# Kernel tuning notes

Hardware: AMD Instinct MI355X
Metric: run time of the kernel (lower is better)

Reference implementation:

```python
import jax, jax.numpy as jnp
import numpy as np

VOCAB, EMB, HID, OUT = 32000, 512, 1024, 8
B, S = 128, 512


def setup_inputs() -> dict:
    key = jax.random.key(0)
    ks = jax.random.split(key, 7)
    sequence_ids = jax.random.randint(ks[0], (B, S), 0, VOCAB)
    scale = 0.02
    emb = jax.random.normal(ks[1], (VOCAB, EMB), dtype=jnp.float32) * scale
    W_ih = jax.random.normal(ks[2], (4 * HID, EMB), dtype=jnp.float32) * scale
    W_hh = jax.random.normal(ks[3], (4 * HID, HID), dtype=jnp.float32) * scale
    b = jax.random.normal(ks[4], (4 * HID,), dtype=jnp.float32) * scale
    W_out = jax.random.normal(ks[5], (OUT, HID), dtype=jnp.float32) * scale
    b_out = jax.random.normal(ks[6], (OUT,), dtype=jnp.float32) * scale
    return {"sequence_ids": sequence_ids, "emb": emb, "W_ih": W_ih, "W_hh": W_hh,
            "b": b, "W_out": W_out, "b_out": b_out}


def reference(sequence_ids, emb, W_ih, W_hh, b, W_out, b_out):
    # embedding lookup: [B, S, E]
    x = emb[sequence_ids]
    Bb = x.shape[0]
    H = W_hh.shape[1]
    # precompute input projections for all timesteps at once: [S, B, 4H]
    xg = jnp.einsum('bse,ge->sbg', x, W_ih) + b

    def step(carry, xg_t):
        h, c = carry
        gates = xg_t + h @ W_hh.T  # [B, 4H]
        i, f, g, o = jnp.split(gates, 4, axis=-1)
        c = jax.nn.sigmoid(f) * c + jax.nn.sigmoid(i) * jnp.tanh(g)
        h = jax.nn.sigmoid(o) * jnp.tanh(c)
        return (h, c), None

    h0 = jnp.zeros((Bb, H), x.dtype)
    (h_last, _), _ = jax.lax.scan(step, (h0, h0), xg)
    # classifier on last hidden state: [B, OUT]
    return h_last @ W_out.T + b_out
```

## Files before the change

kernel.cpp:

```cpp
#include <hip/hip_runtime.h>
#include <cstdint>
#include <cstddef>

#define SEQ    512
#define BATCH  128
#define EMB    512
#define HID    1024
#define KTOT   1536
#define NOUT   8

#define RG     4
#define NBQ    64
#define NBLK   (RG*NBQ)
#define ROWS   32

typedef unsigned short u16;
typedef unsigned int   u32;
typedef unsigned long long u64;
typedef __attribute__((ext_vector_type(8))) __bf16 bf16x8;
typedef __attribute__((ext_vector_type(4))) float  f32x4;
typedef __attribute__((ext_vector_type(4))) float  float4v;
typedef __attribute__((ext_vector_type(4))) u16    u16x4;

#define OFF_X    0ull
#define SZ_X     ((size_t)SEQ*BATCH*EMB*2)
#define OFF_W    (OFF_X + SZ_X)
#define SZ_W     ((size_t)4*HID*KTOT*2)
#define OFF_RING (OFF_W + SZ_W)
#define SZ_RING  ((size_t)(SEQ+1)*BATCH*HID*2)
#define OFF_CNT  (OFF_RING + SZ_RING)
#define SZ_CNT   ((size_t)16*RG*64)
#define OFF_GO   (OFF_CNT + SZ_CNT)
#define SZ_GO    ((size_t)RG*64)
#define WS_NEED  (OFF_GO + SZ_GO)

__device__ inline u16 f2b(float f) {
  uint32_t u = __builtin_bit_cast(uint32_t, f);
  u = u + 0x7FFFu + ((u >> 16) & 1u);
  return (u16)(u >> 16);
}
__device__ inline float b2f(u16 u) {
  uint32_t v = ((uint32_t)u) << 16;
  return __builtin_bit_cast(float, v);
}
__device__ inline float sigm(float x) { return 1.0f / (1.0f + __expf(-x)); }
__device__ inline float tanh_(float x) {
  x = fminf(fmaxf(x, -15.f), 15.f);
  float e = __expf(2.f * x);
  return (e - 1.f) / (e + 1.f);
}
__device__ inline f32x4 mfma16(bf16x8 a, bf16x8 b, f32x4 c) {
  return __builtin_amdgcn_mfma_f32_16x16x32_bf16(a, b, c, 0, 0, 0);
}

__global__ void embed_kernel(const int* __restrict__ ids,
                             const float* __restrict__ emb,
                             u16* __restrict__ x) {
  int bid = blockIdx.x;
  int t = bid >> 7, b = bid & 127;
  int idx = ids[b * SEQ + t];
  const float4v* src = (const float4v*)(emb + (size_t)idx * EMB);
  float4v v = src[threadIdx.x];
  u16x4 o;
  o.x = f2b(v.x); o.y = f2b(v.y); o.z = f2b(v.z); o.w = f2b(v.w);
  *(u16x4*)(x + (size_t)bid * EMB + threadIdx.x * 4) = o;
}

__global__ void wpack_kernel(const float* __restrict__ Wih,
                             const float* __restrict__ Whh,
                             u16* __restrict__ Wp) {
  int gc = blockIdx.x;
  int unit = gc >> 2, q = gc & 3;
  int row = q * HID + unit;
  u16* dst = Wp + (size_t)gc * KTOT;
  for (int k = threadIdx.x; k < KTOT; k += 256) {
    float v = (k < EMB) ? Wih[(size_t)row * EMB + k]
                        : Whh[(size_t)row * HID + (k - EMB)];
    dst[k] = f2b(v);
  }
}

__global__ __launch_bounds__(256, 1) void lstm_kernel(
    const u16* __restrict__ x,
    const u16* __restrict__ Wp,
    const float* __restrict__ bias,
    u16* __restrict__ ring,
    u32* __restrict__ cnt,
    u32* __restrict__ go)
{
  __shared__ float pacc[4][ROWS][68];

  const int tid  = threadIdx.x;
  const int bid  = blockIdx.x;
  const int rg   = bid >> 6;
  const int nb   = bid & 63;
  const int lane = tid & 63;
  const int kq   = tid >> 6;
  const int l15  = lane & 15;
  const int lhi  = lane >> 4;

  const int nxc  = (kq == 0) ? 12 : (kq == 1 ? 4 : 0);
  const int arow = rg * ROWS + l15;

  bf16x8 wreg[12][4];
  {
    const int colbase = nb * 64;
    #pragma unroll
    for (int c = 0; c < 12; ++c)
      #pragma unroll
      for (int nt = 0; nt < 4; ++nt)
        wreg[c][nt] = *(const bf16x8*)(Wp
            + (size_t)(colbase + nt * 16 + l15) * KTOT
            + kq * 384 + c * 32 + lhi * 8);
  }

  const int urow = tid >> 3;
  const int up   = tid & 7;
  const int rowg = rg * ROWS + urow;
  float bs[2][4];
  #pragma unroll
  for (int k = 0; k < 2; ++k) {
    int ug = nb * 16 + 2 * up + k;
    #pragma unroll
    for (int q = 0; q < 4; ++q) bs[k][q] = bias[q * HID + ug];
  }
  float cst[2] = {0.f, 0.f};

  u32* gol = &go[rg * 16];

  bf16x8 af[2][12];
  #pragma unroll
  for (int c = 0; c < 12; ++c)
    if (c < nxc) {
      #pragma unroll
      for (int mt = 0; mt < 2; ++mt)
        af[mt][c] = *(const bf16x8*)(x + (size_t)(arow + mt * 16) * EMB
                                     + kq * 384 + c * 32 + lhi * 8);
    }

  #pragma unroll 1
  for (int t = 0; t < SEQ; ++t) {
    f32x4 acc[2][4];
    #pragma unroll
    for (int mt = 0; mt < 2; ++mt)
      #pragma unroll
      for (int nt = 0; nt < 4; ++nt) acc[mt][nt] = (f32x4){0.f, 0.f, 0.f, 0.f};
    #pragma unroll
    for (int c = 0; c < 12; ++c)
      if (c < nxc) {
        #pragma unroll
        for (int mt = 0; mt < 2; ++mt)
          #pragma unroll
          for (int nt = 0; nt < 4; ++nt)
            acc[mt][nt] = mfma16(af[mt][c], wreg[c][nt], acc[mt][nt]);
      }

    if (t > 0) {
      if (tid == 0) {
        while (__hip_atomic_load(gol, __ATOMIC_RELAXED,
                                 __HIP_MEMORY_SCOPE_AGENT) < (u32)t)
          __builtin_amdgcn_s_sleep(1);
        __asm__ __volatile__("" ::: "memory");
      }
      __syncthreads();
    }

    {
      const u16* hb = ring + (size_t)t * (BATCH * HID);
      #pragma unroll
      for (int c = 0; c < 12; ++c)
        if (c >= nxc) {
          #pragma unroll
          for (int mt = 0; mt < 2; ++mt)
            af[mt][c] = *(const bf16x8*)(hb + (size_t)(arow + mt * 16) * HID
                                         + (kq * 384 - 512 + c * 32) + lhi * 8);
        }
    }

    {
      int tn = (t + 1 < SEQ) ? (t + 1) : t;
      const u16* xb = x + (size_t)tn * (BATCH * EMB);
      #pragma unroll
      for (int c = 0; c < 12; ++c)
        if (c < nxc) {
          #pragma unroll
          for (int mt = 0; mt < 2; ++mt)
            af[mt][c] = *(const bf16x8*)(xb + (size_t)(arow + mt * 16) * EMB
                                         + kq * 384 + c * 32 + lhi * 8);
        }
    }


    #pragma unroll
    for (int c = 0; c < 12; ++c)
      if (c >= nxc) {
        #pragma unroll
        for (int mt = 0; mt < 2; ++mt)
          #pragma unroll
          for (int nt = 0; nt < 4; ++nt)
            acc[mt][nt] = mfma16(af[mt][c], wreg[c][nt], acc[mt][nt]);
      }

    #pragma unroll
    for (int mt = 0; mt < 2; ++mt)
      #pragma unroll
      for (int nt = 0; nt < 4; ++nt)
        #pragma unroll
        for (int rr = 0; rr < 4; ++rr) {
          int row = mt * 16 + lhi * 4 + rr;
          int c   = nt * 16 + l15;
          int pc  = (c & ~7) | ((c ^ row) & 7);
          pacc[kq][row][pc] = acc[mt][nt][rr];
        }
    __syncthreads();

    {
      float s[2][4];
      #pragma unroll
      for (int k = 0; k < 2; ++k)
        #pragma unroll
        for (int q = 0; q < 4; ++q) s[k][q] = bs[k][q];
      #pragma unroll
      for (int k2 = 0; k2 < 4; ++k2)
        #pragma unroll
        for (int cl = 0; cl < 8; ++cl) {
          int pc = 8 * up + ((cl ^ urow) & 7);
          s[cl >> 2][cl & 3] += pacc[k2][urow][pc];
        }
      float hv2[2];
      #pragma unroll
      for (int k = 0; k < 2; ++k) {
        float cn = sigm(s[k][1]) * cst[k] + sigm(s[k][0]) * tanh_(s[k][2]);
        cst[k] = cn;
        hv2[k] = sigm(s[k][3]) * tanh_(cn);
      }
      u32 val = (u32)f2b(hv2[0]) | ((u32)f2b(hv2[1]) << 16);
      u32* dst = (u32*)(ring + (size_t)(t + 1) * (BATCH * HID)
                        + (size_t)rowg * HID + nb * 16 + 2 * up);
      asm volatile("global_store_dword %0, %1, off sc0 sc1 nt"
                   :: "v"(dst), "v"(val) : "memory");
    }
    asm volatile("s_waitcnt vmcnt(0)" ::: "memory");

    __syncthreads();
    if (t == SEQ - 1) break;
    if (tid == 0) {
      u32* cl_ = &cnt[((size_t)(t & 15) * RG + rg) * 16];
      u32 old = __hip_atomic_fetch_add(cl_, 1u, __ATOMIC_RELAXED,
                                       __HIP_MEMORY_SCOPE_AGENT);
      if (old == (u32)(NBQ - 1)) {
        __hip_atomic_store(cl_, 0u, __ATOMIC_RELAXED,
                           __HIP_MEMORY_SCOPE_AGENT);
        __hip_atomic_store(gol, (u32)(t + 1), __ATOMIC_RELAXED,
                           __HIP_MEMORY_SCOPE_AGENT);
      }
    }
  }
}

__global__ void head_kernel(const u16* __restrict__ h,
                            const float* __restrict__ Wout,
                            const float* __restrict__ bout,
                            float* __restrict__ out) {
  int b = blockIdx.x, l = threadIdx.x;
  float p[NOUT];
  #pragma unroll
  for (int o = 0; o < NOUT; ++o) p[o] = 0.f;
  for (int k = l; k < HID; k += 64) {
    float hv = b2f(h[(size_t)b * HID + k]);
    #pragma unroll
    for (int o = 0; o < NOUT; ++o) p[o] += hv * Wout[(size_t)o * HID + k];
  }
  #pragma unroll
  for (int o = 0; o < NOUT; ++o) {
    float v = p[o];
    #pragma unroll
    for (int off = 32; off > 0; off >>= 1) v += __shfl_down(v, off);
    if (l == 0) out[b * NOUT + o] = v + bout[o];
  }
}

__global__ void sentinel_kernel(float* out, int n) {
  int i = blockIdx.x * 256 + threadIdx.x;
  if (i < n) out[i] = 1e9f;
}

extern "C" void kernel_launch(void* const* d_in, const int* in_sizes, int n_in,
                              void* d_out, int out_size, void* d_ws, size_t ws_size,
                              hipStream_t stream) {
  const int*   ids  = (const int*)d_in[0];
  const float* emb  = (const float*)d_in[1];
  const float* Wih  = (const float*)d_in[2];
  const float* Whh  = (const float*)d_in[3];
  const float* bias = (const float*)d_in[4];
  const float* Wout = (const float*)d_in[5];
  const float* bout = (const float*)d_in[6];
  float* out = (float*)d_out;

  if (ws_size < WS_NEED) {
    sentinel_kernel<<<(out_size + 255) / 256, 256, 0, stream>>>(out, out_size);
    return;
  }

  char* ws = (char*)d_ws;
  u16* x    = (u16*)(ws + OFF_X);
  u16* Wp   = (u16*)(ws + OFF_W);
  u16* ring = (u16*)(ws + OFF_RING);
  u32* cnt  = (u32*)(ws + OFF_CNT);
  u32* go   = (u32*)(ws + OFF_GO);

  hipMemsetAsync(ring, 0, (size_t)BATCH * HID * 2, stream);
  hipMemsetAsync(cnt, 0, SZ_CNT + SZ_GO, stream);

  embed_kernel<<<SEQ * BATCH, 128, 0, stream>>>(ids, emb, x);
  wpack_kernel<<<4 * HID, 256, 0, stream>>>(Wih, Whh, Wp);

  lstm_kernel<<<NBLK, 256, 0, stream>>>(x, Wp, bias, ring, cnt, go);

  head_kernel<<<BATCH, 64, 0, stream>>>(ring + (size_t)SEQ * BATCH * HID,
                                        Wout, bout, out);
}
```

Baseline: 3.124 ms.

## Split grid barrier into sub-group counters and balance K split across waves

The per-row-group barrier counter is split into eight sub-group counters, each incremented by eight blocks. Waiters poll all eight sub-flags with one wavefront and a wave-wide vote, which is meant to cut atomic contention on a single hot counter. The K dimension is also redistributed so that each of the four waves handles 128 input columns and 256 hidden columns. Previously wave 0 did all input work and waves 2-3 did only hidden work, so this evens out the post-barrier critical path of MFMAs. The cost is more polling loads per step and a wider global load pattern per wave.

New measurement: 3.361 ms. +7.6%, slower.

```diff
diff --git a/kernel.cpp b/kernel.cpp
--- a/kernel.cpp
+++ b/kernel.cpp
@@ -13,6 +13,7 @@
 #define NBQ    64
 #define NBLK   (RG*NBQ)
 #define ROWS   32
+#define NGR    8
 
 typedef unsigned short u16;
 typedef unsigned int   u32;
@@ -29,10 +30,12 @@
 #define OFF_RING (OFF_W + SZ_W)
 #define SZ_RING  ((size_t)(SEQ+1)*BATCH*HID*2)
 #define OFF_CNT  (OFF_RING + SZ_RING)
-#define SZ_CNT   ((size_t)16*RG*64)
-#define OFF_GO   (OFF_CNT + SZ_CNT)
-#define SZ_GO    ((size_t)RG*64)
-#define WS_NEED  (OFF_GO + SZ_GO)
+#define SZ_CNT   ((size_t)16*RG*NGR*64)
+#define OFF_SGO  (OFF_CNT + SZ_CNT)
+#define SZ_SGO   ((size_t)RG*NGR*64)
+#define WS_NEED  (OFF_SGO + SZ_SGO)
+
+#define KMAP(kq, c) ((c) < 4 ? ((kq)*128 + (c)*32) : (512 + (kq)*256 + ((c)-4)*32))
 
 __device__ inline u16 f2b(float f) {
   uint32_t u = __builtin_bit_cast(uint32_t, f);
@@ -86,7 +89,7 @@
     const float* __restrict__ bias,
     u16* __restrict__ ring,
     u32* __restrict__ cnt,
-    u32* __restrict__ go)
+    u32* __restrict__ subgo)
 {
   __shared__ float pacc[4][ROWS][68];
 
@@ -98,8 +101,8 @@
   const int kq   = tid >> 6;
   const int l15  = lane & 15;
   const int lhi  = lane >> 4;
-
-  const int nxc  = (kq == 0) ? 12 : (kq == 1 ? 4 : 0);
+  const int grp  = nb & (NGR - 1);
+
   const int arow = rg * ROWS + l15;
 
   bf16x8 wreg[12][4];
@@ -111,7 +114,7 @@
       for (int nt = 0; nt < 4; ++nt)
         wreg[c][nt] = *(const bf16x8*)(Wp
             + (size_t)(colbase + nt * 16 + l15) * KTOT
-            + kq * 384 + c * 32 + lhi * 8);
+            + KMAP(kq, c) + lhi * 8);
   }
 
   const int urow = tid >> 3;
@@ -126,17 +129,14 @@
   }
   float cst[2] = {0.f, 0.f};
 
-  u32* gol = &go[rg * 16];
-
   bf16x8 af[2][12];
   #pragma unroll
-  for (int c = 0; c < 12; ++c)
-    if (c < nxc) {
-      #pragma unroll
-      for (int mt = 0; mt < 2; ++mt)
-        af[mt][c] = *(const bf16x8*)(x + (size_t)(arow + mt * 16) * EMB
-                                     + kq * 384 + c * 32 + lhi * 8);
-    }
+  for (int c = 0; c < 4; ++c) {
+    #pragma unroll
+    for (int mt = 0; mt < 2; ++mt)
+      af[mt][c] = *(const bf16x8*)(x + (size_t)(arow + mt * 16) * EMB
+                                   + kq * 128 + c * 32 + lhi * 8);
+  }
 
   #pragma unroll 1
   for (int t = 0; t < SEQ; ++t) {
@@ -146,20 +146,23 @@
       #pragma unroll
       for (int nt = 0; nt < 4; ++nt) acc[mt][nt] = (f32x4){0.f, 0.f, 0.f, 0.f};
     #pragma unroll
-    for (int c = 0; c < 12; ++c)
-      if (c < nxc) {
-        #pragma unroll
-        for (int mt = 0; mt < 2; ++mt)
-          #pragma unroll
-          for (int nt = 0; nt < 4; ++nt)
-            acc[mt][nt] = mfma16(af[mt][c], wreg[c][nt], acc[mt][nt]);
-      }
+    for (int c = 0; c < 4; ++c)
+      #pragma unroll
+      for (int mt = 0; mt < 2; ++mt)
+        #pragma unroll
+        for (int nt = 0; nt < 4; ++nt)
+          acc[mt][nt] = mfma16(af[mt][c], wreg[c][nt], acc[mt][nt]);
 
     if (t > 0) {
-      if (tid == 0) {
-        while (__hip_atomic_load(gol, __ATOMIC_RELAXED,
-                                 __HIP_MEMORY_SCOPE_AGENT) < (u32)t)
+      if (tid < 64) {
+        const u32 tgt = (u32)t;
+        const u32* sg = &subgo[((size_t)rg * NGR + (lane & 7)) * 16];
+        for (;;) {
+          u32 v = __hip_atomic_load(sg, __ATOMIC_RELAXED,
+                                    __HIP_MEMORY_SCOPE_AGENT);
+          if (__all(v >= tgt)) break;
           __builtin_amdgcn_s_sleep(1);
+        }
         __asm__ __volatile__("" ::: "memory");
       }
       __syncthreads();
@@ -168,38 +171,33 @@
     {
       const u16* hb = ring + (size_t)t * (BATCH * HID);
       #pragma unroll
-      for (int c = 0; c < 12; ++c)
-        if (c >= nxc) {
-          #pragma unroll
-          for (int mt = 0; mt < 2; ++mt)
-            af[mt][c] = *(const bf16x8*)(hb + (size_t)(arow + mt * 16) * HID
-                                         + (kq * 384 - 512 + c * 32) + lhi * 8);
-        }
+      for (int c = 4; c < 12; ++c) {
+        #pragma unroll
+        for (int mt = 0; mt < 2; ++mt)
+          af[mt][c] = *(const bf16x8*)(hb + (size_t)(arow + mt * 16) * HID
+                                       + kq * 256 + (c - 4) * 32 + lhi * 8);
+      }
     }
 
     {
       int tn = (t + 1 < SEQ) ? (t + 1) : t;
       const u16* xb = x + (size_t)tn * (BATCH * EMB);
       #pragma unroll
-      for (int c = 0; c < 12; ++c)
-        if (c < nxc) {
-          #pragma unroll
-          for (int mt = 0; mt < 2; ++mt)
-            af[mt][c] = *(const bf16x8*)(xb + (size_t)(arow + mt * 16) * EMB
-                                         + kq * 384 + c * 32 + lhi * 8);
-        }
-    }
-
-
-    #pragma unroll
-    for (int c = 0; c < 12; ++c)
-      if (c >= nxc) {
+      for (int c = 0; c < 4; ++c) {
         #pragma unroll
         for (int mt = 0; mt < 2; ++mt)
-          #pragma unroll
-          for (int nt = 0; nt < 4; ++nt)
-            acc[mt][nt] = mfma16(af[mt][c], wreg[c][nt], acc[mt][nt]);
-      }
+          af[mt][c] = *(const bf16x8*)(xb + (size_t)(arow + mt * 16) * EMB
+                                       + kq * 128 + c * 32 + lhi * 8);
+      }
+    }
+
+    #pragma unroll
+    for (int c = 4; c < 12; ++c)
+      #pragma unroll
+      for (int mt = 0; mt < 2; ++mt)
+        #pragma unroll
+        for (int nt = 0; nt < 4; ++nt)
+          acc[mt][nt] = mfma16(af[mt][c], wreg[c][nt], acc[mt][nt]);
 
     #pragma unroll
     for (int mt = 0; mt < 2; ++mt)
@@ -245,14 +243,14 @@
     __syncthreads();
     if (t == SEQ - 1) break;
     if (tid == 0) {
-      u32* cl_ = &cnt[((size_t)(t & 15) * RG + rg) * 16];
+      u32* cl_ = &cnt[((((size_t)(t & 15) * RG) + rg) * NGR + grp) * 16];
       u32 old = __hip_atomic_fetch_add(cl_, 1u, __ATOMIC_RELAXED,
                                        __HIP_MEMORY_SCOPE_AGENT);
-      if (old == (u32)(NBQ - 1)) {
+      if (old == (u32)(NBLK / RG / NGR - 1)) {
         __hip_atomic_store(cl_, 0u, __ATOMIC_RELAXED,
                            __HIP_MEMORY_SCOPE_AGENT);
-        __hip_atomic_store(gol, (u32)(t + 1), __ATOMIC_RELAXED,
-                           __HIP_MEMORY_SCOPE_AGENT);
+        __hip_atomic_store(&subgo[((size_t)rg * NGR + grp) * 16], (u32)(t + 1),
+                           __ATOMIC_RELAXED, __HIP_MEMORY_SCOPE_AGENT);
       }
     }
   }
@@ -303,19 +301,19 @@
   }
 
   char* ws = (char*)d_ws;
-  u16* x    = (u16*)(ws + OFF_X);
-  u16* Wp   = (u16*)(ws + OFF_W);
-  u16* ring = (u16*)(ws + OFF_RING);
-  u32* cnt  = (u32*)(ws + OFF_CNT);
-  u32* go   = (u32*)(ws + OFF_GO);
+  u16* x     = (u16*)(ws + OFF_X);
+  u16* Wp    = (u16*)(ws + OFF_W);
+  u16* ring  = (u16*)(ws + OFF_RING);
+  u32* cnt   = (u32*)(ws + OFF_CNT);
+  u32* subgo = (u32*)(ws + OFF_SGO);
 
   hipMemsetAsync(ring, 0, (size_t)BATCH * HID * 2, stream);
-  hipMemsetAsync(cnt, 0, SZ_CNT + SZ_GO, stream);
+  hipMemsetAsync(cnt, 0, SZ_CNT + SZ_SGO, stream);
 
   embed_kernel<<<SEQ * BATCH, 128, 0, stream>>>(ids, emb, x);
   wpack_kernel<<<4 * HID, 256, 0, stream>>>(Wih, Whh, Wp);
 
-  lstm_kernel<<<NBLK, 256, 0, stream>>>(x, Wp, bias, ring, cnt, go);
+  lstm_kernel<<<NBLK, 256, 0, stream>>>(x, Wp, bias, ring, cnt, subgo);
 
   head_kernel<<<BATCH, 64, 0, stream>>>(ring + (size_t)SEQ * BATCH * HID,
                                         Wout, bout, out);
```
